# Optimization experiments

Measured on AMD Instinct MI355X. Metric: run time of the kernel, lower is better.

Reference implementation:

```python
import jax, jax.numpy as jnp
import numpy as np

B, H, L, D = 8, 8, 2048, 512

def setup_inputs() -> dict:
    key = jax.random.key(0)
    k1, k2 = jax.random.split(key)
    x = jax.random.normal(k1, (B, H, L, D), dtype=jnp.float32)
    mask = jnp.ones((B, L), dtype=jnp.int32)  # unused by the layer's call()
    complex_weight = 0.02 * jax.random.normal(k2, (H, L, D, 2), dtype=jnp.float32)
    return {"x": x, "mask": mask, "complex_weight": complex_weight}

def reference(x, mask, complex_weight):
    # FFT over the innermost (model_size) axis, matching tf.signal.fft
    fft_x = jnp.fft.fft(x.astype(jnp.complex64), axis=-1)
    w = jax.lax.complex(complex_weight[..., 0], complex_weight[..., 1])  # (H, L, D)
    gated = w * fft_x  # broadcast over batch
    out = jnp.fft.ifft(gated, axis=-1).real.astype(jnp.float32)
    return out
```

## Files before the change

kernel.cpp:

```cpp
#include <hip/hip_runtime.h>
#include <math.h>


#define HL 16384

__device__ __forceinline__ float2 cadd(float2 a, float2 b){ return make_float2(a.x+b.x, a.y+b.y); }
__device__ __forceinline__ float2 csub(float2 a, float2 b){ return make_float2(a.x-b.x, a.y-b.y); }
__device__ __forceinline__ float2 cmul(float2 a, float2 b){ return make_float2(a.x*b.x - a.y*b.y, a.x*b.y + a.y*b.x); }

__device__ __forceinline__ float2 twiddle(float f) {
    return make_float2(__builtin_amdgcn_cosf(f), -__builtin_amdgcn_sinf(f));
}

__device__ __forceinline__ void lds_order() {
    __builtin_amdgcn_wave_barrier();
}

__device__ __forceinline__ void fft8(float2 x[8]) {
    const float c = 0.70710678118654752f;
    float2 u0 = cadd(x[0], x[4]);
    float2 u1 = cadd(x[1], x[5]);
    float2 u2 = cadd(x[2], x[6]);
    float2 u3 = cadd(x[3], x[7]);
    float2 v0 = csub(x[0], x[4]);
    float2 t1 = csub(x[1], x[5]);
    float2 t2 = csub(x[2], x[6]);
    float2 t3 = csub(x[3], x[7]);
    float2 v1 = make_float2(c*(t1.x + t1.y), c*(t1.y - t1.x));
    float2 v2 = make_float2(t2.y, -t2.x);
    float2 v3 = make_float2(c*(t3.y - t3.x), -c*(t3.x + t3.y));
    float2 p0 = cadd(u0, u2), p1 = cadd(u1, u3);
    float2 q0 = csub(u0, u2), q1t = csub(u1, u3);
    float2 q1 = make_float2(q1t.y, -q1t.x);
    x[0] = cadd(p0, p1);
    x[4] = csub(p0, p1);
    x[2] = cadd(q0, q1);
    x[6] = csub(q0, q1);
    float2 r0 = cadd(v0, v2), r1 = cadd(v1, v3);
    float2 s0 = csub(v0, v2), s1t = csub(v1, v3);
    float2 s1 = make_float2(s1t.y, -s1t.x);
    x[1] = cadd(r0, r1);
    x[5] = csub(r0, r1);
    x[3] = cadd(s0, s1);
    x[7] = csub(s0, s1);
}

__device__ __forceinline__ void fft512_r(float2 v[8], int role, int lane, float2* sc,
                                         const float2 tw2[8])
{
    fft8(v);
    {
        const float2 w1 = twiddle((float)role * (1.0f/512.0f));
        const float2 w2 = cmul(w1, w1);
        const float2 w3 = cmul(w1, w2);
        const float2 w4 = cmul(w2, w2);
        const float2 w5 = cmul(w1, w4);
        const float2 w6 = cmul(w2, w4);
        const float2 w7 = cmul(w3, w4);
        v[1] = cmul(v[1], w1);
        v[2] = cmul(v[2], w2);
        v[3] = cmul(v[3], w3);
        v[4] = cmul(v[4], w4);
        v[5] = cmul(v[5], w5);
        v[6] = cmul(v[6], w6);
        v[7] = cmul(v[7], w7);
    }
    lds_order();
    #pragma unroll
    for (int k1 = 0; k1 < 8; ++k1) sc[k1*72 + role] = v[k1];
    lds_order();
    const int k1 = lane >> 3, m2 = lane & 7;
    float2 u[8];
    #pragma unroll
    for (int m1 = 0; m1 < 8; ++m1) u[m1] = sc[k1*72 + 8*m1 + m2];
    fft8(u);
    #pragma unroll
    for (int j = 1; j < 8; ++j) u[j] = cmul(u[j], tw2[j]);
    lds_order();
    #pragma unroll
    for (int j1 = 0; j1 < 8; ++j1) sc[k1*72 + 9*j1 + m2] = u[j1];
    lds_order();
    const int j1 = lane & 7;
    #pragma unroll
    for (int m = 0; m < 8; ++m) v[m] = sc[k1*72 + 9*j1 + m];
    fft8(v);
}

using gu32 = __attribute__((address_space(1))) const unsigned int;
using lu32 = __attribute__((address_space(3))) unsigned int;

__global__ __launch_bounds__(256, 4) void sgn_fft_diet(
    const float* __restrict__ x,
    const float* __restrict__ cw,
    float* __restrict__ out)
{
    __shared__ __align__(16) float2 sc[4][8*72];
    __shared__ __align__(16) float  xb[4][2][512];

    const int tid  = threadIdx.x;
    const int wid  = tid >> 6;
    const int lane = tid & 63;
    const int dsl  = ((lane & 7) << 3) | (lane >> 3);
    const int hl   = blockIdx.x;

    const int r1 = (wid       * HL + hl) * 512;
    const int r2 = ((wid + 4) * HL + hl) * 512;

    #pragma unroll
    for (int c = 0; c < 2; ++c) {
        __builtin_amdgcn_global_load_lds((gu32*)(x + r1 + c*256 + 4*lane),
                                         (lu32*)(&xb[wid][0][c*256]), 16, 0, 0);
        __builtin_amdgcn_global_load_lds((gu32*)(x + r2 + c*256 + 4*lane),
                                         (lu32*)(&xb[wid][1][c*256]), 16, 0, 0);
    }
    __builtin_amdgcn_sched_barrier(0);

    float2 tw2[8];
    {
        const int m2 = lane & 7;
        tw2[1] = twiddle((float)m2 * (1.0f/64.0f));
        tw2[2] = cmul(tw2[1], tw2[1]);
        tw2[3] = cmul(tw2[1], tw2[2]);
        tw2[4] = cmul(tw2[2], tw2[2]);
        tw2[5] = cmul(tw2[1], tw2[4]);
        tw2[6] = cmul(tw2[2], tw2[4]);
        tw2[7] = cmul(tw2[3], tw2[4]);
    }

    const float2* __restrict__ cw2 = (const float2*)cw;
    const int wrow = hl * 512;
    float2 wk[8], wnk[8];
    #pragma unroll
    for (int j2 = 0; j2 < 8; ++j2) {
        const int k  = dsl + 64*j2;
        const int nk = (512 - k) & 511;
        wk[j2]  = cw2[wrow + k];
        wnk[j2] = cw2[wrow + nk];
    }

    asm volatile("s_waitcnt vmcnt(16)" ::: "memory");

    float2 v[8];
    #pragma unroll
    for (int j = 0; j < 8; ++j) {
        v[j].x = xb[wid][0][64*j + lane];
        v[j].y = xb[wid][1][64*j + lane];
    }

    float2* scw = &sc[wid][0];
    fft512_r(v, lane, lane, scw, tw2);

    {
        const float hs = 0.5f / 512.0f;
        #pragma unroll
        for (int j2 = 0; j2 < 8; ++j2) {
            const float2 wp = make_float2(hs*(wk[j2].x + wnk[j2].x),
                                          hs*(wk[j2].y - wnk[j2].y));
            const float2 g  = cmul(wp, v[j2]);
            v[j2] = make_float2(g.x, -g.y);
        }
    }

    fft512_r(v, dsl, lane, scw, tw2);

    lds_order();
    {
        float2* OD = scw;
        #pragma unroll
        for (int j2 = 0; j2 < 8; ++j2)
            OD[dsl + 64*j2] = make_float2(v[j2].x, -v[j2].y);
    }
    lds_order();
    #pragma unroll
    for (int c = 0; c < 2; ++c) {
        const float2* OD = scw;
        const float4 p = *(const float4*)&OD[4*lane + 256*c];
        const float4 q = *(const float4*)&OD[4*lane + 256*c + 2];
        *(float4*)(out + r1 + 4*lane + 256*c) = make_float4(p.x, p.z, q.x, q.z);
        *(float4*)(out + r2 + 4*lane + 256*c) = make_float4(p.y, p.w, q.y, q.w);
    }
}

extern "C" void kernel_launch(void* const* d_in, const int* in_sizes, int n_in,
                              void* d_out, int out_size, void* d_ws, size_t ws_size,
                              hipStream_t stream) {
    const float* x  = (const float*)d_in[0];
    const float* cw = (const float*)d_in[2];
    float* out = (float*)d_out;

    sgn_fft_diet<<<dim3(HL), dim3(256), 0, stream>>>(x, cw, out);
}
```

Measured before the change: 477.4 us.

## Make blocks persistent over eight rows with double-buffered prefetch of next inputs

Each block now processes eight consecutive (h,l) rows instead of one, with the grid reduced to 2048 blocks. While the current row is being transformed, the next row's x data is prefetched into LDS via global_load_lds and the next weight values into alternating register sets. This is meant to hide global-load latency and amortise per-block setup such as twiddle computation. The mirrored-weight loads are now issued inline, and the single LDS x buffer is reused with manual waitcnt ordering, which risks subtle races and leaves fewer blocks to spread across CUs.

```diff
diff --git a/kernel.cpp b/kernel.cpp
--- a/kernel.cpp
+++ b/kernel.cpp
@@ -2,7 +2,9 @@
 #include <math.h>
 
 
-#define HL 16384
+#define HL    16384
+#define NBLK  2048
+#define ITERS 8
 
 __device__ __forceinline__ float2 cadd(float2 a, float2 b){ return make_float2(a.x+b.x, a.y+b.y); }
 __device__ __forceinline__ float2 csub(float2 a, float2 b){ return make_float2(a.x-b.x, a.y-b.y); }
@@ -89,7 +91,70 @@
 using gu32 = __attribute__((address_space(1))) const unsigned int;
 using lu32 = __attribute__((address_space(3))) unsigned int;
 
-__global__ __launch_bounds__(256, 4) void sgn_fft_diet(
+#define BODY(T, WKC, WKN)                                                          \
+{                                                                                  \
+    const int hl   = hlb + (T);                                                    \
+    const int r1   = (wid       * HL + hl) * 512;                                  \
+    const int r2   = ((wid + 4) * HL + hl) * 512;                                  \
+    const int wrow = hl * 512;                                                     \
+               \
+    asm volatile("s_waitcnt vmcnt(8)" ::: "memory");                               \
+    float2 v[8];                                                                   \
+    _Pragma("unroll")                                                              \
+    for (int j = 0; j < 8; ++j) {                                                  \
+        v[j].x = xb[wid][0][64*j + lane];                                          \
+        v[j].y = xb[wid][1][64*j + lane];                                          \
+    }                                                                              \
+                        \
+    asm volatile("s_waitcnt lgkmcnt(0)" ::: "memory");                             \
+    lds_order();                                                                   \
+    if ((T) + 1 < ITERS) {                                                         \
+        const int r1n = r1 + 512, r2n = r2 + 512;                        \
+        _Pragma("unroll")                                                          \
+        for (int c = 0; c < 2; ++c) {                                              \
+            __builtin_amdgcn_global_load_lds((gu32*)(x + r1n + c*256 + 4*lane),    \
+                                             (lu32*)(&xb[wid][0][c*256]), 16,0,0); \
+            __builtin_amdgcn_global_load_lds((gu32*)(x + r2n + c*256 + 4*lane),    \
+                                             (lu32*)(&xb[wid][1][c*256]), 16,0,0); \
+        }                                                                          \
+    }                                                                              \
+    fft512_r(v, lane, lane, scw, tw2);                                             \
+       \
+    {                                                                              \
+        const float hs = 0.5f / 512.0f;                                            \
+        _Pragma("unroll")                                                          \
+        for (int j2 = 0; j2 < 8; ++j2) {                                           \
+            const int k  = dsl + 64*j2;                                            \
+            const int nk = (512 - k) & 511;                                        \
+            const float2 wnk = cw2[wrow + nk];                                     \
+            const float2 wp  = make_float2(hs*(WKC[j2].x + wnk.x),                 \
+                                           hs*(WKC[j2].y - wnk.y));                \
+            const float2 g   = cmul(wp, v[j2]);                                    \
+            v[j2] = make_float2(g.x, -g.y);                                        \
+        }                                                                          \
+    }                                                                              \
+    if ((T) + 1 < ITERS) {                                                         \
+        _Pragma("unroll")                                                          \
+        for (int j2 = 0; j2 < 8; ++j2)                                             \
+            WKN[j2] = cw2[wrow + 512 + dsl + 64*j2];                               \
+    }                                                                              \
+    fft512_r(v, dsl, lane, scw, tw2);                                              \
+                      \
+    lds_order();                                                                   \
+    _Pragma("unroll")                                                              \
+    for (int j2 = 0; j2 < 8; ++j2)                                                 \
+        scw[dsl + 64*j2] = make_float2(v[j2].x, -v[j2].y);                         \
+    lds_order();                                                                   \
+    _Pragma("unroll")                                                              \
+    for (int c = 0; c < 2; ++c) {                                                  \
+        const float4 p = *(const float4*)&scw[4*lane + 256*c];                     \
+        const float4 q = *(const float4*)&scw[4*lane + 256*c + 2];                 \
+        *(float4*)(out + r1 + 4*lane + 256*c) = make_float4(p.x, p.z, q.x, q.z);   \
+        *(float4*)(out + r2 + 4*lane + 256*c) = make_float4(p.y, p.w, q.y, q.w);   \
+    }                                                                              \
+}
+
+__global__ __launch_bounds__(256, 4) void sgn_fft_pp(
     const float* __restrict__ x,
     const float* __restrict__ cw,
     float* __restrict__ out)
@@ -101,19 +166,28 @@
     const int wid  = tid >> 6;
     const int lane = tid & 63;
     const int dsl  = ((lane & 7) << 3) | (lane >> 3);
-    const int hl   = blockIdx.x;
-
-    const int r1 = (wid       * HL + hl) * 512;
-    const int r2 = ((wid + 4) * HL + hl) * 512;
-
-    #pragma unroll
-    for (int c = 0; c < 2; ++c) {
-        __builtin_amdgcn_global_load_lds((gu32*)(x + r1 + c*256 + 4*lane),
-                                         (lu32*)(&xb[wid][0][c*256]), 16, 0, 0);
-        __builtin_amdgcn_global_load_lds((gu32*)(x + r2 + c*256 + 4*lane),
-                                         (lu32*)(&xb[wid][1][c*256]), 16, 0, 0);
-    }
-    __builtin_amdgcn_sched_barrier(0);
+    const int hlb  = blockIdx.x * ITERS;
+
+    const float2* __restrict__ cw2 = (const float2*)cw;
+    float2* scw = &sc[wid][0];
+
+    {
+        const int r1 = (wid       * HL + hlb) * 512;
+        const int r2 = ((wid + 4) * HL + hlb) * 512;
+        #pragma unroll
+        for (int c = 0; c < 2; ++c) {
+            __builtin_amdgcn_global_load_lds((gu32*)(x + r1 + c*256 + 4*lane),
+                                             (lu32*)(&xb[wid][0][c*256]), 16, 0, 0);
+            __builtin_amdgcn_global_load_lds((gu32*)(x + r2 + c*256 + 4*lane),
+                                             (lu32*)(&xb[wid][1][c*256]), 16, 0, 0);
+        }
+    }
+    float2 wkA[8], wkB[8];
+    {
+        const int wrow = hlb * 512;
+        #pragma unroll
+        for (int j2 = 0; j2 < 8; ++j2) wkA[j2] = cw2[wrow + dsl + 64*j2];
+    }
 
     float2 tw2[8];
     {
@@ -127,58 +201,14 @@
         tw2[7] = cmul(tw2[3], tw2[4]);
     }
 
-    const float2* __restrict__ cw2 = (const float2*)cw;
-    const int wrow = hl * 512;
-    float2 wk[8], wnk[8];
-    #pragma unroll
-    for (int j2 = 0; j2 < 8; ++j2) {
-        const int k  = dsl + 64*j2;
-        const int nk = (512 - k) & 511;
-        wk[j2]  = cw2[wrow + k];
-        wnk[j2] = cw2[wrow + nk];
-    }
-
-    asm volatile("s_waitcnt vmcnt(16)" ::: "memory");
-
-    float2 v[8];
-    #pragma unroll
-    for (int j = 0; j < 8; ++j) {
-        v[j].x = xb[wid][0][64*j + lane];
-        v[j].y = xb[wid][1][64*j + lane];
-    }
-
-    float2* scw = &sc[wid][0];
-    fft512_r(v, lane, lane, scw, tw2);
-
-    {
-        const float hs = 0.5f / 512.0f;
-        #pragma unroll
-        for (int j2 = 0; j2 < 8; ++j2) {
-            const float2 wp = make_float2(hs*(wk[j2].x + wnk[j2].x),
-                                          hs*(wk[j2].y - wnk[j2].y));
-            const float2 g  = cmul(wp, v[j2]);
-            v[j2] = make_float2(g.x, -g.y);
-        }
-    }
-
-    fft512_r(v, dsl, lane, scw, tw2);
-
-    lds_order();
-    {
-        float2* OD = scw;
-        #pragma unroll
-        for (int j2 = 0; j2 < 8; ++j2)
-            OD[dsl + 64*j2] = make_float2(v[j2].x, -v[j2].y);
-    }
-    lds_order();
-    #pragma unroll
-    for (int c = 0; c < 2; ++c) {
-        const float2* OD = scw;
-        const float4 p = *(const float4*)&OD[4*lane + 256*c];
-        const float4 q = *(const float4*)&OD[4*lane + 256*c + 2];
-        *(float4*)(out + r1 + 4*lane + 256*c) = make_float4(p.x, p.z, q.x, q.z);
-        *(float4*)(out + r2 + 4*lane + 256*c) = make_float4(p.y, p.w, q.y, q.w);
-    }
+    BODY(0, wkA, wkB)
+    BODY(1, wkB, wkA)
+    BODY(2, wkA, wkB)
+    BODY(3, wkB, wkA)
+    BODY(4, wkA, wkB)
+    BODY(5, wkB, wkA)
+    BODY(6, wkA, wkB)
+    BODY(7, wkB, wkA)
 }
 
 extern "C" void kernel_launch(void* const* d_in, const int* in_sizes, int n_in,
@@ -188,5 +218,5 @@
     const float* cw = (const float*)d_in[2];
     float* out = (float*)d_out;
 
-    sgn_fft_diet<<<dim3(HL), dim3(256), 0, stream>>>(x, cw, out);
-}
+    sgn_fft_pp<<<dim3(NBLK), dim3(256), 0, stream>>>(x, cw, out);
+}
```

Result: slower. 501.0 us (+5.0%).
